# Performance work log

Hardware: AMD Instinct MI355X
Metric: run time of the kernel (lower is better)

## Reference

```python
import jax, jax.numpy as jnp
import numpy as np

EPS = 1e-5

def _bn4(x, g, b, m, v):
    # eval-mode BatchNorm2d on NCHW
    s = g / jnp.sqrt(v + EPS)
    return x * s[None, :, None, None] + (b - m * s)[None, :, None, None]

def _bn1(x, g, b, m, v):
    # eval-mode BatchNorm over channel dim of (B, C)
    s = g / jnp.sqrt(v + EPS)
    return x * s[None, :] + (b - m * s)[None, :]

def _dw(x, w, pad):
    # depthwise conv, NCHW, weight (C,1,k,k)
    return jax.lax.conv_general_dilated(
        x, w, (1, 1), [(pad, pad), (pad, pad)],
        dimension_numbers=('NCHW', 'OIHW', 'NCHW'),
        feature_group_count=x.shape[1])

def setup_inputs() -> dict:
    key = jax.random.key(0)
    ks = jax.random.split(key, 32)
    B, C, H, W = 64, 96, 56, 56
    d = {}
    d['x'] = jax.random.normal(ks[0], (B, C, H, W), jnp.float32)
    d['w3'] = jax.random.normal(ks[1], (C, 1, 3, 3), jnp.float32) * 0.2
    d['g3'] = jax.random.normal(ks[2], (C,), jnp.float32)
    d['b3'] = jax.random.normal(ks[3], (C,), jnp.float32)
    d['m3'] = jax.random.normal(ks[4], (C,), jnp.float32)
    d['v3'] = jax.random.uniform(ks[5], (C,), jnp.float32)
    d['w5'] = jax.random.normal(ks[6], (C, 1, 5, 5), jnp.float32) * 0.2
    d['g5'] = jax.random.normal(ks[7], (C,), jnp.float32)
    d['b5'] = jax.random.normal(ks[8], (C,), jnp.float32)
    d['m5'] = jax.random.normal(ks[9], (C,), jnp.float32)
    d['v5'] = jax.random.uniform(ks[10], (C,), jnp.float32)
    d['w1'] = jax.random.normal(ks[11], (C, 1, 1, 1), jnp.float32) * 0.2
    d['b1'] = jax.random.normal(ks[12], (C,), jnp.float32) * 0.1
    d['gbn'] = jax.random.normal(ks[13], (C,), jnp.float32)
    d['bbn'] = jax.random.normal(ks[14], (C,), jnp.float32)
    d['mbn'] = jax.random.normal(ks[15], (C,), jnp.float32)
    d['vbn'] = jax.random.uniform(ks[16], (C,), jnp.float32)
    d['kw1'] = jax.random.normal(ks[17], (4, C), jnp.float32) * 0.1
    d['kg1'] = jax.random.normal(ks[18], (4,), jnp.float32)
    d['kb1'] = jax.random.normal(ks[19], (4,), jnp.float32)
    d['km1'] = jax.random.normal(ks[20], (4,), jnp.float32)
    d['kv1'] = jax.random.uniform(ks[21], (4,), jnp.float32)
    d['kw2'] = jax.random.normal(ks[22], (2, 4), jnp.float32) * 0.1
    d['kg2'] = jax.random.normal(ks[23], (2,), jnp.float32)
    d['kb2'] = jax.random.normal(ks[24], (2,), jnp.float32)
    d['km2'] = jax.random.normal(ks[25], (2,), jnp.float32)
    d['kv2'] = jax.random.uniform(ks[26], (2,), jnp.float32)
    return d

def reference(x, w3, g3, b3, m3, v3, w5, g5, b5, m5, v5, w1, b1,
              gbn, bbn, mbn, vbn,
              kw1, kg1, kb1, km1, kv1, kw2, kg2, kb2, km2, kv2):
    # kernel_predictor: GAP -> 1x1 conv+BN -> GELU -> 1x1 conv+BN -> softmax
    pooled = x.mean(axis=(2, 3))                      # (B, C)
    h = _bn1(pooled @ kw1.T, kg1, kb1, km1, kv1)      # (B, 4)
    h = jax.nn.gelu(h, approximate=False)
    h = _bn1(h @ kw2.T, kg2, kb2, km2, kv2)           # (B, 2)
    kwts = jax.nn.softmax(h, axis=1)
    # both branches computed batched, then per-sample selection mask
    y3 = _bn4(_dw(x, w3, 1), g3, b3, m3, v3)
    y5 = _bn4(_dw(x, w5, 2), g5, b5, m5, v5)
    sel = (kwts[:, 0] > kwts[:, 1])[:, None, None, None]
    y1 = _dw(x, w1, 0) + b1[None, :, None, None]      # conv1 has a bias
    out = _bn4(jnp.where(sel, y3, y5) + y1, gbn, bbn, mbn, vbn)
    return out
```

## Files before the change

kernel.cpp:

```cpp
#include <hip/hip_runtime.h>
#include <math.h>

#define EPS 1e-5f


__global__ __launch_bounds__(256) void pool_kernel(const float* __restrict__ x,
                                                   float* __restrict__ pooled) {
    const int bc = blockIdx.x;
    const float4* xp4 = (const float4*)(x + (size_t)bc * 3136);
    const int tid = threadIdx.x;
    float s = 0.f;
    for (int i = tid; i < 784; i += 256) {
        float4 v = xp4[i];
        s += (v.x + v.y) + (v.z + v.w);
    }
    for (int off = 32; off > 0; off >>= 1)
        s += __shfl_down(s, off, 64);
    __shared__ float wsum[4];
    if ((tid & 63) == 0) wsum[tid >> 6] = s;
    __syncthreads();
    if (tid == 0) {
        float t = (wsum[0] + wsum[1]) + (wsum[2] + wsum[3]);
        pooled[bc] = t * (1.f / 3136.f);
    }
}

__global__ __launch_bounds__(64) void sel_kernel(
    const float* __restrict__ pooled,
    const float* __restrict__ kw1, const float* __restrict__ kg1,
    const float* __restrict__ kb1, const float* __restrict__ km1,
    const float* __restrict__ kv1,
    const float* __restrict__ kw2, const float* __restrict__ kg2,
    const float* __restrict__ kb2, const float* __restrict__ km2,
    const float* __restrict__ kv2,
    int* __restrict__ sel) {
    const int b = threadIdx.x;
    const float* p = pooled + b * 96;
    double h1[4];
#pragma unroll
    for (int j = 0; j < 4; ++j) {
        double acc = 0.0;
        for (int c = 0; c < 96; ++c)
            acc += (double)p[c] * (double)kw1[j * 96 + c];
        double s = (double)kg1[j] / sqrt((double)kv1[j] + 1e-5);
        double h = acc * s + ((double)kb1[j] - (double)km1[j] * s);
        h1[j] = h * 0.5 * (1.0 + erf(h * 0.70710678118654752440));
    }
    double h2[2];
#pragma unroll
    for (int k = 0; k < 2; ++k) {
        double acc = 0.0;
#pragma unroll
        for (int j = 0; j < 4; ++j) acc += h1[j] * (double)kw2[k * 4 + j];
        double s = (double)kg2[k] / sqrt((double)kv2[k] + 1e-5);
        h2[k] = acc * s + ((double)kb2[k] - (double)km2[k] * s);
    }
    sel[b] = (h2[0] > h2[1]) ? 1 : 0;
}

template <int K>
__device__ __forceinline__ void conv_tile(const float (&f)[8][8],
                                          const float (&wg)[K * K],
                                          float (&acc)[4][4]) {
    constexpr int off = (K == 3) ? 1 : 0;
#pragma unroll
    for (int yy = 0; yy < 4; ++yy) {
#pragma unroll
        for (int ky = 0; ky < K; ++ky) {
#pragma unroll
            for (int kx = 0; kx < K; ++kx) {
                const float w = wg[ky * K + kx];
#pragma unroll
                for (int j = 0; j < 4; ++j)
                    acc[yy][j] = fmaf(w, f[yy + ky + off][j + kx + off], acc[yy][j]);
            }
        }
    }
}

__global__ __launch_bounds__(256) void fused_conv_kernel(
    const float* __restrict__ x,
    const float* __restrict__ w3, const float* __restrict__ g3,
    const float* __restrict__ b3, const float* __restrict__ m3,
    const float* __restrict__ v3,
    const float* __restrict__ w5, const float* __restrict__ g5,
    const float* __restrict__ b5, const float* __restrict__ m5,
    const float* __restrict__ v5,
    const float* __restrict__ w1, const float* __restrict__ b1,
    const float* __restrict__ gbn, const float* __restrict__ bbn,
    const float* __restrict__ mbn, const float* __restrict__ vbn,
    const int* __restrict__ sel,
    float* __restrict__ out) {
    __shared__ float lds[60 * 64];
    const int bc = blockIdx.x;
    const int b = bc / 96;
    const int c = bc - b * 96;
    const int tid = threadIdx.x;

    for (int i = tid; i < 60 * 64; i += 256) lds[i] = 0.f;
    __syncthreads();
    const float4* xp4 = (const float4*)(x + (size_t)bc * 3136);
    for (int i = tid; i < 784; i += 256) {
        float4 v = xp4[i];
        const int y = i / 14;
        const int xq = i - y * 14;
        float2* dst = (float2*)&lds[(y + 2) * 64 + 2 + xq * 4];
        dst[0] = make_float2(v.x, v.y);
        dst[1] = make_float2(v.z, v.w);
    }
    __syncthreads();

    if (tid >= 196) return;
    const int rb = tid / 14;
    const int q = tid - rb * 14;
    const int x0 = q * 4, y0 = rb * 4;

    float f[8][8];
#pragma unroll
    for (int r = 0; r < 8; ++r) {
        const float4* p = (const float4*)&lds[(y0 + r) * 64 + q * 4];
        float4 a = p[0], bb = p[1];
        f[r][0] = a.x;  f[r][1] = a.y;  f[r][2] = a.z;  f[r][3] = a.w;
        f[r][4] = bb.x; f[r][5] = bb.y; f[r][6] = bb.z; f[r][7] = bb.w;
    }

    const float sbn = gbn[c] * rsqrtf(vbn[c] + EPS);
    const float tbn = bbn[c] - mbn[c] * sbn;
    const float w1c = sbn * w1[c];
    const float b1c = b1[c];

    float acc[4][4];
    if (sel[b]) {
        const float sk = g3[c] * rsqrtf(v3[c] + EPS);
        const float A = sbn * sk;
        const float Cc = sbn * ((b3[c] - m3[c] * sk) + b1c) + tbn;
        float wg[9];
#pragma unroll
        for (int i = 0; i < 9; ++i) wg[i] = A * w3[c * 9 + i];
        wg[4] += w1c;
#pragma unroll
        for (int yy = 0; yy < 4; ++yy)
#pragma unroll
            for (int j = 0; j < 4; ++j) acc[yy][j] = Cc;
        conv_tile<3>(f, wg, acc);
    } else {
        const float sk = g5[c] * rsqrtf(v5[c] + EPS);
        const float A = sbn * sk;
        const float Cc = sbn * ((b5[c] - m5[c] * sk) + b1c) + tbn;
        float wg[25];
#pragma unroll
        for (int i = 0; i < 25; ++i) wg[i] = A * w5[c * 25 + i];
        wg[12] += w1c;
#pragma unroll
        for (int yy = 0; yy < 4; ++yy)
#pragma unroll
            for (int j = 0; j < 4; ++j) acc[yy][j] = Cc;
        conv_tile<5>(f, wg, acc);
    }

    float* op = out + (size_t)bc * 3136;
#pragma unroll
    for (int yy = 0; yy < 4; ++yy) {
        float4 v = make_float4(acc[yy][0], acc[yy][1], acc[yy][2], acc[yy][3]);
        *(float4*)(op + (y0 + yy) * 56 + x0) = v;
    }
}

extern "C" void kernel_launch(void* const* d_in, const int* in_sizes, int n_in,
                              void* d_out, int out_size, void* d_ws, size_t ws_size,
                              hipStream_t stream) {
    const float* x   = (const float*)d_in[0];
    const float* w3  = (const float*)d_in[1];
    const float* g3  = (const float*)d_in[2];
    const float* b3  = (const float*)d_in[3];
    const float* m3  = (const float*)d_in[4];
    const float* v3  = (const float*)d_in[5];
    const float* w5  = (const float*)d_in[6];
    const float* g5  = (const float*)d_in[7];
    const float* b5  = (const float*)d_in[8];
    const float* m5  = (const float*)d_in[9];
    const float* v5  = (const float*)d_in[10];
    const float* w1  = (const float*)d_in[11];
    const float* b1  = (const float*)d_in[12];
    const float* gbn = (const float*)d_in[13];
    const float* bbn = (const float*)d_in[14];
    const float* mbn = (const float*)d_in[15];
    const float* vbn = (const float*)d_in[16];
    const float* kw1 = (const float*)d_in[17];
    const float* kg1 = (const float*)d_in[18];
    const float* kb1 = (const float*)d_in[19];
    const float* km1 = (const float*)d_in[20];
    const float* kv1 = (const float*)d_in[21];
    const float* kw2 = (const float*)d_in[22];
    const float* kg2 = (const float*)d_in[23];
    const float* kb2 = (const float*)d_in[24];
    const float* km2 = (const float*)d_in[25];
    const float* kv2 = (const float*)d_in[26];
    float* out = (float*)d_out;

    float* pooled = (float*)d_ws;
    int* sel = (int*)((char*)d_ws + 6144 * sizeof(float));

    pool_kernel<<<6144, 256, 0, stream>>>(x, pooled);
    sel_kernel<<<1, 64, 0, stream>>>(pooled, kw1, kg1, kb1, km1, kv1,
                                     kw2, kg2, kb2, km2, kv2, sel);
    fused_conv_kernel<<<6144, 256, 0, stream>>>(
        x, w3, g3, b3, m3, v3, w5, g5, b5, m5, v5, w1, b1,
        gbn, bbn, mbn, vbn, sel, out);
}
```

Baseline: 219.9 us.

## Fuse pooling with selector via last-block counter and restructure conv as sliding-row loads

The pool and selector kernels are merged into one kernel, where the last block to finish, found through an atomic counter, runs the small MLP. This removes a launch and the idle tail of a single-block kernel, at the cost of a memset and atomics. The conv kernel drops the LDS staging. Each thread now handles a 4-wide column strip over 14 rows, reading rows straight from global memory into a rolling 5-row register window, with 3x3 weights zero-padded to 5x5. That gives up the cheaper 3x3 arithmetic path, and neighbouring threads load overlapping data redundantly, in exchange for no shared memory, no barriers and more useful threads per block.

```diff
diff --git a/kernel.cpp b/kernel.cpp
--- a/kernel.cpp
+++ b/kernel.cpp
@@ -4,29 +4,9 @@
 #define EPS 1e-5f
 
 
-__global__ __launch_bounds__(256) void pool_kernel(const float* __restrict__ x,
-                                                   float* __restrict__ pooled) {
-    const int bc = blockIdx.x;
-    const float4* xp4 = (const float4*)(x + (size_t)bc * 3136);
-    const int tid = threadIdx.x;
-    float s = 0.f;
-    for (int i = tid; i < 784; i += 256) {
-        float4 v = xp4[i];
-        s += (v.x + v.y) + (v.z + v.w);
-    }
-    for (int off = 32; off > 0; off >>= 1)
-        s += __shfl_down(s, off, 64);
-    __shared__ float wsum[4];
-    if ((tid & 63) == 0) wsum[tid >> 6] = s;
-    __syncthreads();
-    if (tid == 0) {
-        float t = (wsum[0] + wsum[1]) + (wsum[2] + wsum[3]);
-        pooled[bc] = t * (1.f / 3136.f);
-    }
-}
-
-__global__ __launch_bounds__(64) void sel_kernel(
-    const float* __restrict__ pooled,
+__global__ __launch_bounds__(256) void pool_sel_kernel(
+    const float* __restrict__ x,
+    float* __restrict__ pooled, unsigned* __restrict__ counter,
     const float* __restrict__ kw1, const float* __restrict__ kg1,
     const float* __restrict__ kb1, const float* __restrict__ km1,
     const float* __restrict__ kv1,
@@ -34,51 +14,67 @@
     const float* __restrict__ kb2, const float* __restrict__ km2,
     const float* __restrict__ kv2,
     int* __restrict__ sel) {
-    const int b = threadIdx.x;
-    const float* p = pooled + b * 96;
-    double h1[4];
-#pragma unroll
-    for (int j = 0; j < 4; ++j) {
-        double acc = 0.0;
-        for (int c = 0; c < 96; ++c)
-            acc += (double)p[c] * (double)kw1[j * 96 + c];
-        double s = (double)kg1[j] / sqrt((double)kv1[j] + 1e-5);
-        double h = acc * s + ((double)kb1[j] - (double)km1[j] * s);
-        h1[j] = h * 0.5 * (1.0 + erf(h * 0.70710678118654752440));
-    }
-    double h2[2];
-#pragma unroll
-    for (int k = 0; k < 2; ++k) {
-        double acc = 0.0;
-#pragma unroll
-        for (int j = 0; j < 4; ++j) acc += h1[j] * (double)kw2[k * 4 + j];
-        double s = (double)kg2[k] / sqrt((double)kv2[k] + 1e-5);
-        h2[k] = acc * s + ((double)kb2[k] - (double)km2[k] * s);
-    }
-    sel[b] = (h2[0] > h2[1]) ? 1 : 0;
+    __shared__ float smem[6208];
+    __shared__ float wsum[4];
+    __shared__ int lastflag;
+    const int bc = blockIdx.x;
+    const int tid = threadIdx.x;
+
+    const float4* xp4 = (const float4*)(x + (size_t)bc * 3136);
+    float s = 0.f;
+    for (int i = tid; i < 784; i += 256) {
+        float4 v = xp4[i];
+        s += (v.x + v.y) + (v.z + v.w);
+    }
+    for (int off = 32; off > 0; off >>= 1) s += __shfl_down(s, off, 64);
+    if ((tid & 63) == 0) wsum[tid >> 6] = s;
+    __syncthreads();
+    if (tid == 0) {
+        float t = (wsum[0] + wsum[1]) + (wsum[2] + wsum[3]);
+        __hip_atomic_store(&pooled[bc], t * (1.f / 3136.f),
+                           __ATOMIC_RELEASE, __HIP_MEMORY_SCOPE_AGENT);
+        __threadfence();
+        unsigned old = __hip_atomic_fetch_add(counter, 1u, __ATOMIC_ACQ_REL,
+                                              __HIP_MEMORY_SCOPE_AGENT);
+        lastflag = (old == (unsigned)(gridDim.x - 1));
+    }
+    __syncthreads();
+    if (!lastflag) return;
+
+    __threadfence();
+    for (int i = tid; i < 6144; i += 256) {
+        float v = __hip_atomic_load(&pooled[i], __ATOMIC_RELAXED,
+                                    __HIP_MEMORY_SCOPE_AGENT);
+        int bb = i / 96;
+        smem[bb * 97 + (i - bb * 96)] = v;
+    }
+    __syncthreads();
+    if (tid < 64) {
+        const float* p = &smem[tid * 97];
+        double h1[4];
+#pragma unroll
+        for (int j = 0; j < 4; ++j) {
+            double acc = 0.0;
+            for (int c = 0; c < 96; ++c)
+                acc += (double)p[c] * (double)kw1[j * 96 + c];
+            double sg = (double)kg1[j] / sqrt((double)kv1[j] + 1e-5);
+            double h = acc * sg + ((double)kb1[j] - (double)km1[j] * sg);
+            h1[j] = h * 0.5 * (1.0 + erf(h * 0.70710678118654752440));
+        }
+        double h2[2];
+#pragma unroll
+        for (int k = 0; k < 2; ++k) {
+            double acc = 0.0;
+#pragma unroll
+            for (int j = 0; j < 4; ++j) acc += h1[j] * (double)kw2[k * 4 + j];
+            double sg = (double)kg2[k] / sqrt((double)kv2[k] + 1e-5);
+            h2[k] = acc * sg + ((double)kb2[k] - (double)km2[k] * sg);
+        }
+        sel[tid] = (h2[0] > h2[1]) ? 1 : 0;
+    }
 }
 
-template <int K>
-__device__ __forceinline__ void conv_tile(const float (&f)[8][8],
-                                          const float (&wg)[K * K],
-                                          float (&acc)[4][4]) {
-    constexpr int off = (K == 3) ? 1 : 0;
-#pragma unroll
-    for (int yy = 0; yy < 4; ++yy) {
-#pragma unroll
-        for (int ky = 0; ky < K; ++ky) {
-#pragma unroll
-            for (int kx = 0; kx < K; ++kx) {
-                const float w = wg[ky * K + kx];
-#pragma unroll
-                for (int j = 0; j < 4; ++j)
-                    acc[yy][j] = fmaf(w, f[yy + ky + off][j + kx + off], acc[yy][j]);
-            }
-        }
-    }
-}
-
-__global__ __launch_bounds__(256) void fused_conv_kernel(
+__global__ __launch_bounds__(256) void conv_kernel(
     const float* __restrict__ x,
     const float* __restrict__ w3, const float* __restrict__ g3,
     const float* __restrict__ b3, const float* __restrict__ m3,
@@ -89,80 +85,81 @@
     const float* __restrict__ w1, const float* __restrict__ b1,
     const float* __restrict__ gbn, const float* __restrict__ bbn,
     const float* __restrict__ mbn, const float* __restrict__ vbn,
-    const int* __restrict__ sel,
-    float* __restrict__ out) {
-    __shared__ float lds[60 * 64];
-    const int bc = blockIdx.x;
+    const int* __restrict__ sel, float* __restrict__ out) {
+    const int t = blockIdx.x * 256 + threadIdx.x;
+    const int q = t % 14;
+    const int r = t / 14;
+    const int ys = r & 3;
+    const int bc = r >> 2;
     const int b = bc / 96;
     const int c = bc - b * 96;
-    const int tid = threadIdx.x;
-
-    for (int i = tid; i < 60 * 64; i += 256) lds[i] = 0.f;
-    __syncthreads();
-    const float4* xp4 = (const float4*)(x + (size_t)bc * 3136);
-    for (int i = tid; i < 784; i += 256) {
-        float4 v = xp4[i];
-        const int y = i / 14;
-        const int xq = i - y * 14;
-        float2* dst = (float2*)&lds[(y + 2) * 64 + 2 + xq * 4];
-        dst[0] = make_float2(v.x, v.y);
-        dst[1] = make_float2(v.z, v.w);
-    }
-    __syncthreads();
-
-    if (tid >= 196) return;
-    const int rb = tid / 14;
-    const int q = tid - rb * 14;
-    const int x0 = q * 4, y0 = rb * 4;
-
-    float f[8][8];
-#pragma unroll
-    for (int r = 0; r < 8; ++r) {
-        const float4* p = (const float4*)&lds[(y0 + r) * 64 + q * 4];
-        float4 a = p[0], bb = p[1];
-        f[r][0] = a.x;  f[r][1] = a.y;  f[r][2] = a.z;  f[r][3] = a.w;
-        f[r][4] = bb.x; f[r][5] = bb.y; f[r][6] = bb.z; f[r][7] = bb.w;
-    }
+    const int y0 = ys * 14;
+    const float* __restrict__ base = x + (size_t)bc * 3136;
 
     const float sbn = gbn[c] * rsqrtf(vbn[c] + EPS);
     const float tbn = bbn[c] - mbn[c] * sbn;
-    const float w1c = sbn * w1[c];
-    const float b1c = b1[c];
-
-    float acc[4][4];
+    float wg[25];
+    float Cc;
     if (sel[b]) {
         const float sk = g3[c] * rsqrtf(v3[c] + EPS);
         const float A = sbn * sk;
-        const float Cc = sbn * ((b3[c] - m3[c] * sk) + b1c) + tbn;
-        float wg[9];
-#pragma unroll
-        for (int i = 0; i < 9; ++i) wg[i] = A * w3[c * 9 + i];
-        wg[4] += w1c;
-#pragma unroll
-        for (int yy = 0; yy < 4; ++yy)
-#pragma unroll
-            for (int j = 0; j < 4; ++j) acc[yy][j] = Cc;
-        conv_tile<3>(f, wg, acc);
+#pragma unroll
+        for (int i = 0; i < 25; ++i) wg[i] = 0.f;
+#pragma unroll
+        for (int ky = 0; ky < 3; ++ky)
+#pragma unroll
+            for (int kx = 0; kx < 3; ++kx)
+                wg[(ky + 1) * 5 + (kx + 1)] = A * w3[c * 9 + ky * 3 + kx];
+        Cc = sbn * ((b3[c] - m3[c] * sk) + b1[c]) + tbn;
     } else {
         const float sk = g5[c] * rsqrtf(v5[c] + EPS);
         const float A = sbn * sk;
-        const float Cc = sbn * ((b5[c] - m5[c] * sk) + b1c) + tbn;
-        float wg[25];
 #pragma unroll
         for (int i = 0; i < 25; ++i) wg[i] = A * w5[c * 25 + i];
-        wg[12] += w1c;
-#pragma unroll
-        for (int yy = 0; yy < 4; ++yy)
-#pragma unroll
-            for (int j = 0; j < 4; ++j) acc[yy][j] = Cc;
-        conv_tile<5>(f, wg, acc);
-    }
-
-    float* op = out + (size_t)bc * 3136;
-#pragma unroll
-    for (int yy = 0; yy < 4; ++yy) {
-        float4 v = make_float4(acc[yy][0], acc[yy][1], acc[yy][2], acc[yy][3]);
-        *(float4*)(op + (y0 + yy) * 56 + x0) = v;
+        Cc = sbn * ((b5[c] - m5[c] * sk) + b1[c]) + tbn;
+    }
+    wg[12] += sbn * w1[c];
+
+    float f[5][8];
+    auto load_row = [&](int row, float* dst) {
+        if ((unsigned)row > 55u) {
+#pragma unroll
+            for (int i = 0; i < 8; ++i) dst[i] = 0.f;
+            return;
+        }
+        const float* rp = base + row * 56;
+        float2 Aa = *(const float2*)(rp + (q > 0 ? 4 * q - 2 : 0));
+        float4 Bv = *(const float4*)(rp + 4 * q);
+        float2 Cv = *(const float2*)(rp + (q < 13 ? 4 * q + 4 : 48));
+        if (q == 0) { Aa.x = 0.f; Aa.y = 0.f; }
+        if (q == 13) { Cv.x = 0.f; Cv.y = 0.f; }
+        dst[0] = Aa.x; dst[1] = Aa.y;
+        dst[2] = Bv.x; dst[3] = Bv.y; dst[4] = Bv.z; dst[5] = Bv.w;
+        dst[6] = Cv.x; dst[7] = Cv.y;
+    };
+
+#pragma unroll
+    for (int i = 0; i < 4; ++i) load_row(y0 - 2 + i, f[i]);
+
+    float* op = out + (size_t)bc * 3136 + y0 * 56 + 4 * q;
+#pragma unroll
+    for (int j = 0; j < 14; ++j) {
+        load_row(y0 + 2 + j, f[(4 + j) % 5]);
+        float a0 = Cc, a1 = Cc, a2 = Cc, a3 = Cc;
+#pragma unroll
+        for (int ky = 0; ky < 5; ++ky) {
+            const float* fr = f[(j + ky) % 5];
+#pragma unroll
+            for (int kx = 0; kx < 5; ++kx) {
+                const float w = wg[ky * 5 + kx];
+                a0 = fmaf(w, fr[kx], a0);
+                a1 = fmaf(w, fr[kx + 1], a1);
+                a2 = fmaf(w, fr[kx + 2], a2);
+                a3 = fmaf(w, fr[kx + 3], a3);
+            }
+        }
+        *(float4*)op = make_float4(a0, a1, a2, a3);
+        op += 56;
     }
 }
 
@@ -198,13 +195,15 @@
     const float* kv2 = (const float*)d_in[26];
     float* out = (float*)d_out;
 
-    float* pooled = (float*)d_ws;
-    int* sel = (int*)((char*)d_ws + 6144 * sizeof(float));
-
-    pool_kernel<<<6144, 256, 0, stream>>>(x, pooled);
-    sel_kernel<<<1, 64, 0, stream>>>(pooled, kw1, kg1, kb1, km1, kv1,
-                                     kw2, kg2, kb2, km2, kv2, sel);
-    fused_conv_kernel<<<6144, 256, 0, stream>>>(
+    unsigned* counter = (unsigned*)d_ws;
+    float* pooled = (float*)d_ws + 64;
+    int* sel = (int*)((float*)d_ws + 64 + 6144);
+
+    hipMemsetAsync(counter, 0, 4, stream);
+    pool_sel_kernel<<<6144, 256, 0, stream>>>(
+        x, pooled, counter, kw1, kg1, kb1, km1, kv1,
+        kw2, kg2, kb2, km2, kv2, sel);
+    conv_kernel<<<1344, 256, 0, stream>>>(
         x, w3, g3, b3, m3, v3, w5, g5, b5, m5, v5, w1, b1,
         gbn, bbn, mbn, vbn, sel, out);
 }
```

Result: slower. 459.3 us (+108.9%).
